# Optimization experiments

Hardware: AMD Instinct MI355X
Metric: run time of the kernel (lower is better)

The kernel has to match this reference:

```python
import jax, jax.numpy as jnp
import numpy as np

B, N, F = 2, 2048, 1024
H, E = 512, 256   # feature_sizes = [1024, 512, 256]
K = 30            # K_max


def setup_inputs() -> dict:
    key = jax.random.key(0)
    k0, k1, k2, k3, k4 = jax.random.split(key, 5)
    x = jax.random.normal(k0, (B, N, F), dtype=jnp.float32)
    s0 = 1.0 / np.sqrt(F)
    s1 = 1.0 / np.sqrt(H)
    # torch.nn.Linear default init: U(-1/sqrt(fan_in), 1/sqrt(fan_in)), weight [out, in]
    W0 = jax.random.uniform(k1, (H, F), jnp.float32, -s0, s0)
    b0 = jax.random.uniform(k2, (H,), jnp.float32, -s0, s0)
    W1 = jax.random.uniform(k3, (E, H), jnp.float32, -s1, s1)
    b1 = jax.random.uniform(k4, (E,), jnp.float32, -s1, s1)
    return {"x": x, "W0": W0, "b0": b0, "W1": W1, "b1": b1}


def _osg_single(xs, W0, b0, W1, b1):
    # xs: [N, F] (no NaNs, so masked_select(~isnan) is identity)
    # DIST (EMBEDDING + cosine)
    h = jax.nn.relu(xs @ W0.T + b0)          # [N, H]
    e = h @ W1.T + b1                         # [N, E]
    corr = e @ e.T                            # [N, N]
    d = jnp.diagonal(corr)                    # [N]
    denom = jnp.sqrt(jnp.clip(d[:, None] * d[None, :], 1e-8, None))
    D = (1.0 - corr / denom) / 2.0            # [N, N]

    # D_SUM_CALC: D_sum[i, j] (j >= i) = sum of D[i:j+1, i:j+1] (block sums)
    # via padded 2D prefix sums. Only the upper triangle is consumed downstream.
    Sp = jnp.pad(jnp.cumsum(jnp.cumsum(D, axis=0), axis=1), ((1, 0), (1, 0)))  # [N+1, N+1]
    dS = jnp.diagonal(Sp)                     # [N+1]
    Bsum = dS[1:][None, :] - Sp[:-1, 1:] - Sp[1:, :-1].T + dS[:-1][:, None]    # [N, N]

    idx = jnp.arange(N)
    BIG = jnp.float32(1e30)
    C0 = Bsum[:, N - 1]                       # C[n, 0] = D_sum[n, N-1]

    # C_TABLE_ALL DP over k, fused with the per-column masked mean:
    # T_pred[i] = mean over all C_all[nn, kk, i] >= 0.
    # k = 0 layer: C_all[n, 0, N-1] = 1 for every n (N entries in column N-1).
    tsum0 = jnp.zeros((N,), jnp.float32).at[N - 1].set(float(N))
    tcnt0 = jnp.zeros((N,), jnp.float32).at[N - 1].set(float(N))

    def step(carry, kk):
        Cprev, tsum, tcnt = carry
        # Cshift[i] = C[i+1, kk-1]; pad value never used (i+1 <= N-kk <= N-1)
        Cshift = jnp.concatenate([Cprev[1:], jnp.zeros((1,), Cprev.dtype)])
        M = Bsum + Cshift[None, :]            # M[nn, i] = D_sum[nn, i] + C[i+1, kk-1]
        valid = (idx[None, :] >= idx[:, None]) & (idx[None, :] < N - kk)  # i in [nn, N-kk)
        Ck = jnp.where(idx < N - kk,
                       jnp.min(jnp.where(valid, M, BIG), axis=1),
                       0.0)                    # torch leaves C at 0 for invalid rows
        soft = jax.nn.softmax(jnp.where(valid, -M, -BIG), axis=1)  # Softmin over valid i
        tsum = tsum + jnp.sum(jnp.where(valid, soft, 0.0), axis=0)
        tcnt = tcnt + jnp.sum(valid, axis=0).astype(tsum.dtype)
        return (Ck, tsum, tcnt), None

    (_, tsum, tcnt), _ = jax.lax.scan(step, (C0, tsum0, tcnt0), jnp.arange(1, K))
    return tsum / tcnt                        # every column has count >= 1 for K >= 2


def reference(x, W0, b0, W1, b1):
    # N == x.shape[1] (no NaN padding needed), so T_out is [B, N]
    return jax.vmap(lambda xs: _osg_single(xs, W0, b0, W1, b1))(x)
```

## Files before the change

### kernel.cpp

```cpp
#include <hip/hip_runtime.h>
#include <hip/hip_bf16.h>
#include <float.h>

#define NTOK 2048
#define FDIM 1024
#define HDIM 512
#define EDIM 256
#define BATCH 2
#define KSEG 30
#define NP1 2049
static const size_t ST2 = (size_t)NP1 * NP1;

__global__ __launch_bounds__(256)
void gemm_nt64(const float* __restrict__ A, int lda,
               const float* __restrict__ Bm, int ldb,
               const float* __restrict__ bias,
               float* __restrict__ C, int ldc, int K)
{
    __shared__ float As[32][68];
    __shared__ float Bs[32][68];
    const int t = threadIdx.x;
    const int tx = t & 15, ty = t >> 4;
    const int lrow = t >> 3, lkv = t & 7;
    const int by = blockIdx.y, bx = blockIdx.x;

    float acc[4][4] = {};
    const int ktiles = K >> 5;
    for (int kt = 0; kt < ktiles; ++kt) {
#pragma unroll
        for (int h = 0; h < 2; ++h) {
            const int r = lrow + h * 32;
            const float4 av = *(const float4*)(A + (size_t)(by * 64 + r) * lda + kt * 32 + lkv * 4);
            As[lkv * 4 + 0][r] = av.x; As[lkv * 4 + 1][r] = av.y;
            As[lkv * 4 + 2][r] = av.z; As[lkv * 4 + 3][r] = av.w;
            const float4 bv = *(const float4*)(Bm + (size_t)(bx * 64 + r) * ldb + kt * 32 + lkv * 4);
            Bs[lkv * 4 + 0][r] = bv.x; Bs[lkv * 4 + 1][r] = bv.y;
            Bs[lkv * 4 + 2][r] = bv.z; Bs[lkv * 4 + 3][r] = bv.w;
        }
        __syncthreads();
#pragma unroll
        for (int kk = 0; kk < 32; ++kk) {
            const float4 a = *(const float4*)&As[kk][ty * 4];
            const float4 b = *(const float4*)&Bs[kk][tx * 4];
            const float ar[4] = {a.x, a.y, a.z, a.w};
            const float br[4] = {b.x, b.y, b.z, b.w};
#pragma unroll
            for (int i = 0; i < 4; ++i)
#pragma unroll
                for (int j = 0; j < 4; ++j)
                    acc[i][j] = fmaf(ar[i], br[j], acc[i][j]);
        }
        __syncthreads();
    }

    const int row0 = by * 64 + ty * 4;
    const int col0 = bx * 64 + tx * 4;
#pragma unroll
    for (int i = 0; i < 4; ++i) {
        float4 v4;
        v4.x = acc[i][0] + bias[col0 + 0];
        v4.y = acc[i][1] + bias[col0 + 1];
        v4.z = acc[i][2] + bias[col0 + 2];
        v4.w = acc[i][3] + bias[col0 + 3];
        *(float4*)(C + (size_t)(row0 + i) * ldc + col0) = v4;
    }
}

__global__ __launch_bounds__(256)
void gemm_nt128s(const float* __restrict__ A, int lda,
                 const float* __restrict__ Bm, int ldb,
                 float* __restrict__ Cp, int ldc, int M, int khalf)
{
    __shared__ float As[16][140];
    __shared__ float Bs[16][140];
    const int t = threadIdx.x;
    const int tx = t & 15, ty = t >> 4;
    const int by = blockIdx.y, bx = blockIdx.x;
    const int k0 = blockIdx.z * khalf;
    const int fq = t & 3, lr = t >> 2;

    float acc[8][8] = {};
    for (int kt = 0; kt < khalf / 16; ++kt) {
#pragma unroll
        for (int h = 0; h < 2; ++h) {
            const int r = lr + h * 64;
            const int rr = r + 4 * (r >> 5);
            const float4 av = *(const float4*)(A + (size_t)(by * 128 + r) * lda + k0 + kt * 16 + fq * 4);
            As[fq * 4 + 0][rr] = av.x; As[fq * 4 + 1][rr] = av.y;
            As[fq * 4 + 2][rr] = av.z; As[fq * 4 + 3][rr] = av.w;
            const float4 bv = *(const float4*)(Bm + (size_t)(bx * 128 + r) * ldb + k0 + kt * 16 + fq * 4);
            Bs[fq * 4 + 0][rr] = bv.x; Bs[fq * 4 + 1][rr] = bv.y;
            Bs[fq * 4 + 2][rr] = bv.z; Bs[fq * 4 + 3][rr] = bv.w;
        }
        __syncthreads();
        const int ma = 8 * ty + 4 * (ty >> 2);
        const int mb = 8 * tx + 4 * (tx >> 2);
#pragma unroll
        for (int k = 0; k < 16; ++k) {
            const float4 a0 = *(const float4*)&As[k][ma];
            const float4 a1 = *(const float4*)&As[k][ma + 4];
            const float4 b0 = *(const float4*)&Bs[k][mb];
            const float4 b1 = *(const float4*)&Bs[k][mb + 4];
            const float ar[8] = {a0.x, a0.y, a0.z, a0.w, a1.x, a1.y, a1.z, a1.w};
            const float br[8] = {b0.x, b0.y, b0.z, b0.w, b1.x, b1.y, b1.z, b1.w};
#pragma unroll
            for (int i = 0; i < 8; ++i)
#pragma unroll
                for (int j = 0; j < 8; ++j)
                    acc[i][j] = fmaf(ar[i], br[j], acc[i][j]);
        }
        __syncthreads();
    }

    float* outp = Cp + (size_t)blockIdx.z * M * ldc;
    const int row0 = by * 128 + ty * 8;
    const int col0 = bx * 128 + tx * 8;
#pragma unroll
    for (int i = 0; i < 8; ++i) {
        float4 w0; w0.x = acc[i][0]; w0.y = acc[i][1]; w0.z = acc[i][2]; w0.w = acc[i][3];
        float4 w1; w1.x = acc[i][4]; w1.y = acc[i][5]; w1.z = acc[i][6]; w1.w = acc[i][7];
        *(float4*)(outp + (size_t)(row0 + i) * ldc + col0) = w0;
        *(float4*)(outp + (size_t)(row0 + i) * ldc + col0 + 4) = w1;
    }
}

__global__ __launch_bounds__(256)
void combine_relu(const float* __restrict__ p0, const float* __restrict__ p1,
                  const float* __restrict__ bias, float* __restrict__ hout)
{
    const int idx = blockIdx.x * 256 + threadIdx.x;
    const float4 a = ((const float4*)p0)[idx];
    const float4 b = ((const float4*)p1)[idx];
    const float4 bs = *(const float4*)&bias[(idx & 127) * 4];
    float4 o;
    o.x = fmaxf(a.x + b.x + bs.x, 0.0f);
    o.y = fmaxf(a.y + b.y + bs.y, 0.0f);
    o.z = fmaxf(a.z + b.z + bs.z, 0.0f);
    o.w = fmaxf(a.w + b.w + bs.w, 0.0f);
    ((float4*)hout)[idx] = o;
}

__global__ __launch_bounds__(256)
void gemm_corr(const float* __restrict__ E, float* __restrict__ D,
               const float* __restrict__ dvec)
{
    __shared__ float As[16][140];
    __shared__ float Bs[16][140];
    const int z = blockIdx.z;
    const float* Eb = E + (size_t)z * NTOK * EDIM;
    float* Db = D + (size_t)z * NTOK * NTOK;
    const int t = threadIdx.x;
    const int tx = t & 15, ty = t >> 4;
    const int by = blockIdx.y, bx = blockIdx.x;
    const int fq = t & 3, lr = t >> 2;

    float acc[8][8] = {};
    for (int kt = 0; kt < EDIM / 16; ++kt) {
#pragma unroll
        for (int h = 0; h < 2; ++h) {
            const int r = lr + h * 64;
            const int rr = r + 4 * (r >> 5);
            const float4 av = *(const float4*)(Eb + (size_t)(by * 128 + r) * EDIM + kt * 16 + fq * 4);
            As[fq * 4 + 0][rr] = av.x; As[fq * 4 + 1][rr] = av.y;
            As[fq * 4 + 2][rr] = av.z; As[fq * 4 + 3][rr] = av.w;
            const float4 bv = *(const float4*)(Eb + (size_t)(bx * 128 + r) * EDIM + kt * 16 + fq * 4);
            Bs[fq * 4 + 0][rr] = bv.x; Bs[fq * 4 + 1][rr] = bv.y;
            Bs[fq * 4 + 2][rr] = bv.z; Bs[fq * 4 + 3][rr] = bv.w;
        }
        __syncthreads();
        const int ma = 8 * ty + 4 * (ty >> 2);
        const int mb = 8 * tx + 4 * (tx >> 2);
#pragma unroll
        for (int k = 0; k < 16; ++k) {
            const float4 a0 = *(const float4*)&As[k][ma];
            const float4 a1 = *(const float4*)&As[k][ma + 4];
            const float4 b0 = *(const float4*)&Bs[k][mb];
            const float4 b1 = *(const float4*)&Bs[k][mb + 4];
            const float ar[8] = {a0.x, a0.y, a0.z, a0.w, a1.x, a1.y, a1.z, a1.w};
            const float br[8] = {b0.x, b0.y, b0.z, b0.w, b1.x, b1.y, b1.z, b1.w};
#pragma unroll
            for (int i = 0; i < 8; ++i)
#pragma unroll
                for (int j = 0; j < 8; ++j)
                    acc[i][j] = fmaf(ar[i], br[j], acc[i][j]);
        }
        __syncthreads();
    }

    const int row0 = by * 128 + ty * 8;
    const int col0 = bx * 128 + tx * 8;
    float di[8], dj[8];
#pragma unroll
    for (int i = 0; i < 8; ++i) di[i] = dvec[z * NTOK + row0 + i];
#pragma unroll
    for (int j = 0; j < 8; ++j) dj[j] = dvec[z * NTOK + col0 + j];
#pragma unroll
    for (int i = 0; i < 8; ++i) {
        float o[8];
#pragma unroll
        for (int j = 0; j < 8; ++j) {
            const float den = sqrtf(fmaxf(di[i] * dj[j], 1e-8f));
            o[j] = 0.5f * (1.0f - acc[i][j] / den);
        }
        float4 w0; w0.x = o[0]; w0.y = o[1]; w0.z = o[2]; w0.w = o[3];
        float4 w1; w1.x = o[4]; w1.y = o[5]; w1.z = o[6]; w1.w = o[7];
        *(float4*)(Db + (size_t)(row0 + i) * NTOK + col0) = w0;
        *(float4*)(Db + (size_t)(row0 + i) * NTOK + col0 + 4) = w1;
    }
}

__global__ __launch_bounds__(256)
void rownorm_kernel(const float* __restrict__ e, float* __restrict__ dvec)
{
    const int wid = (blockIdx.x * 256 + threadIdx.x) >> 6;
    const int lane = threadIdx.x & 63;
    if (wid >= BATCH * NTOK) return;
    const float4 v = *(const float4*)(e + (size_t)wid * EDIM + lane * 4);
    float s = v.x * v.x + v.y * v.y + v.z * v.z + v.w * v.w;
#pragma unroll
    for (int off = 32; off; off >>= 1) s += __shfl_xor(s, off);
    if (lane == 0) dvec[wid] = s;
}

__global__ __launch_bounds__(256)
void sat_row_kernel(const float* __restrict__ D, double* __restrict__ Sp)
{
    const int b = blockIdx.y;
    const int r = blockIdx.x + 1;
    const float* drow = D + (size_t)b * NTOK * NTOK + (size_t)(r - 1) * NTOK;
    double* sprow = Sp + (size_t)b * ST2 + (size_t)r * NP1;
    const int t = threadIdx.x, lane = t & 63, wv = t >> 6;
    __shared__ double wtot[4];
    double carry = 0.0;
    if (t == 0) sprow[0] = 0.0;
    for (int ch = 0; ch < NTOK / 256; ++ch) {
        double v = (double)drow[ch * 256 + t];
#pragma unroll
        for (int d = 1; d < 64; d <<= 1) {
            const double u = __shfl_up(v, (unsigned)d, 64);
            if (lane >= d) v += u;
        }
        if (lane == 63) wtot[wv] = v;
        __syncthreads();
        double pre = carry;
        for (int ww = 0; ww < wv; ++ww) pre += wtot[ww];
        const double tot = carry + wtot[0] + wtot[1] + wtot[2] + wtot[3];
        sprow[ch * 256 + t + 1] = v + pre;
        __syncthreads();
        carry = tot;
    }
}

__global__ void satc1(const double* __restrict__ Sp, double* __restrict__ aux)
{
    const int b = blockIdx.z, s = blockIdx.y;
    const int c = blockIdx.x * 256 + threadIdx.x;
    if (c > NTOK) return;
    const double* sp = Sp + (size_t)b * ST2;
    double tt = 0.0;
    const int r0 = s * 256 + 1;
    for (int r = r0; r < r0 + 256; ++r) tt += sp[(size_t)r * NP1 + c];
    aux[(size_t)(b * 8 + s) * NP1 + c] = tt;
}
__global__ void satc2(double* __restrict__ aux)
{
    const int b = blockIdx.y;
    const int c = blockIdx.x * 256 + threadIdx.x;
    if (c > NTOK) return;
    double run = 0.0;
    for (int s = 0; s < 8; ++s) {
        const size_t id = (size_t)(b * 8 + s) * NP1 + c;
        const double tt = aux[id]; aux[id] = run; run += tt;
    }
}
__global__ void satc3(double* __restrict__ Sp, const double* __restrict__ aux)
{
    const int b = blockIdx.z, s = blockIdx.y;
    const int c = blockIdx.x * 256 + threadIdx.x;
    if (c > NTOK) return;
    double* sp = Sp + (size_t)b * ST2;
    if (s == 0) sp[c] = 0.0;
    double run = aux[(size_t)(b * 8 + s) * NP1 + c];
    const int r0 = s * 256 + 1;
    for (int r = r0; r < r0 + 256; ++r) {
        const size_t id = (size_t)r * NP1 + c;
        run += sp[id];
        sp[id] = run;
    }
}

__global__ void diag_kernel(const double* __restrict__ Sp, double* __restrict__ dg)
{
    const int b = blockIdx.y;
    const int t = blockIdx.x * 256 + threadIdx.x;
    if (t <= NTOK) dg[b * NP1 + t] = Sp[(size_t)b * ST2 + (size_t)t * NP1 + t];
}

__global__ __launch_bounds__(256)
void bsum_kernel(const double* __restrict__ Sp, const double* __restrict__ dg,
                 float* __restrict__ Bsum, float* __restrict__ C0)
{
    const int b = blockIdx.y, i = blockIdx.x;
    const double* sprow = Sp + (size_t)b * ST2 + (size_t)i * NP1;
    const double* dgb = dg + (size_t)b * NP1;
    const double di = dgb[i];
    float* brow = Bsum + (size_t)b * NTOK * NTOK + (size_t)i * NTOK;
    for (int j = i + threadIdx.x; j < NTOK; j += 256) {
        const double v = dgb[j + 1] + di - 2.0 * sprow[j + 1];
        brow[j] = (float)v;
        if (j == NTOK - 1) C0[b * NTOK + i] = (float)v;
    }
}

#define DP_BX 128
#define DP_PAIRS 8
#define RBBIG 3.0e37f

__device__ inline void cstore(float* p, float v)
{
    __hip_atomic_store(p, v, __ATOMIC_RELAXED, __HIP_MEMORY_SCOPE_AGENT);
}

__device__ inline void wait_flags(const int* flagsb, int need)
{
    if (threadIdx.x < DP_BX) {
        const int* f = flagsb + threadIdx.x * 4;
        while (__hip_atomic_load(f, __ATOMIC_RELAXED, __HIP_MEMORY_SCOPE_AGENT) < need)
            __builtin_amdgcn_s_sleep(1);
    }
    __syncthreads();
}

__device__ inline void publish(int* myflag, int val)
{
    asm volatile("s_waitcnt vmcnt(0)" ::: "memory");
    __syncthreads();
    if (threadIdx.x == 0)
        __hip_atomic_store(myflag, val, __ATOMIC_RELAXED, __HIP_MEMORY_SCOPE_AGENT);
}

template<int NC>
__device__ inline void load_rb(const float* __restrict__ brow, int colbase, int lane,
                               float (&rb)[NC])
{
#pragma unroll
    for (int c = 0; c < NC; ++c) {
        const int col = colbase + lane + c * 64;
        rb[c] = (col < NTOK) ? brow[col] : RBBIG;
    }
}

template<int NC>
__device__ inline float pass1(const float (&rb)[NC], const float* __restrict__ cs,
                              int coff, int V, int lane)
{
    float mn = FLT_MAX;
#pragma unroll
    for (int c = 0; c < NC; ++c) {
        const int idx = lane + c * 64;
        if (idx < V) mn = fminf(mn, rb[c] + cs[coff + idx]);
    }
#pragma unroll
    for (int o = 32; o; o >>= 1) mn = fminf(mn, __shfl_xor(mn, o));
    return mn;
}

template<int NC>
__device__ inline void pass2(const float (&rb)[NC], const float* __restrict__ cs,
                             int coff, int V, float mn, int lane, float (&ac)[NC])
{
    float w[NC];
    float s = 0.0f;
#pragma unroll
    for (int c = 0; c < NC; ++c) {
        const int idx = lane + c * 64;
        float x = 0.0f;
        if (idx < V) x = __expf(mn - (rb[c] + cs[coff + idx]));
        w[c] = x;
        s += x;
    }
#pragma unroll
    for (int o = 32; o; o >>= 1) s += __shfl_xor(s, o);
    const float inv = 1.0f / s;
#pragma unroll
    for (int c = 0; c < NC; ++c) ac[c] = __builtin_fmaf(w[c], inv, ac[c]);
}

template<int NC>
__device__ inline void merge_acc(const float (&ac)[NC], int base, int lane,
                                 float* __restrict__ acc_lds)
{
#pragma unroll
    for (int c = 0; c < NC; ++c) {
        const int col = base + lane + c * 64;
        if (col < NTOK && ac[c] != 0.0f) atomicAdd(&acc_lds[col], ac[c]);
    }
}

__global__ __launch_bounds__(256, 1)
void dp_fused_kernel(const float* __restrict__ Bsum,
                     float* __restrict__ Ca, float* __restrict__ Cb,
                     float* __restrict__ tsum, int* __restrict__ flags)
{
    __shared__ float cs[NTOK];
    __shared__ float acc_lds[NTOK];
    const int b = blockIdx.y;
    const int t = threadIdx.x, lane = t & 63, wv = t >> 6;
    const float* Bb = Bsum + (size_t)b * NTOK * NTOK;
    const int pbase = blockIdx.x * DP_PAIRS;
    int* flagsb = flags + b * DP_BX * 4;
    int* myflag = flagsb + blockIdx.x * 4;

    const int p0 = pbase + wv * 2, p1 = p0 + 1;
    const int i1_0 = NTOK - 1 - p0, i1_1 = NTOK - 1 - p1;

    float rbA0[32], rbB0[16], rbA1[32], rbB1[16];
    load_rb<32>(Bb + (size_t)p0 * NTOK, p0, lane, rbA0);
    load_rb<16>(Bb + (size_t)i1_0 * NTOK, i1_0, lane, rbB0);
    load_rb<32>(Bb + (size_t)p1 * NTOK, p1, lane, rbA1);
    load_rb<16>(Bb + (size_t)i1_1 * NTOK, i1_1, lane, rbB1);

    float acA0[32] = {}, acB0[16] = {}, acA1[32] = {}, acB1[16] = {};

    for (int j = t; j < NTOK; j += 256) acc_lds[j] = 0.0f;

    if (t < DP_PAIRS) {
        const int p = pbase + t, i1 = NTOK - 1 - p;
        if (p > 0) cstore(&Ca[b * NTOK + p - 1], Bb[(size_t)p * NTOK + NTOK - 1]);
        cstore(&Ca[b * NTOK + i1 - 1], Bb[(size_t)i1 * NTOK + NTOK - 1]);
    }
    publish(myflag, 0);

    const float* Cr = Ca;
    float* Cn = Cb;

    for (int k = 1; k < KSEG; ++k) {
        wait_flags(flagsb, k - 1);
        {
            const float* base  = Cr + b * NTOK + t * 4;
            const float* base2 = base + 1024;
            float4 va, vb;
            asm volatile(
                "global_load_dwordx4 %0, %2, off sc1\n\t"
                "global_load_dwordx4 %1, %3, off sc1\n\t"
                "s_waitcnt vmcnt(0)"
                : "=&v"(va), "=&v"(vb)
                : "v"(base), "v"(base2)
                : "memory");
            *(float4*)&cs[t * 4] = va;
            *(float4*)&cs[t * 4 + 1024] = vb;
        }
        __syncthreads();
        float* Cnb = Cn + b * NTOK;
        const int jmax = NTOK - k;

        const int VA0 = jmax - p0, VA1 = jmax - p1;
        const int VB0 = p0 + 1 - k, VB1 = p1 + 1 - k;
        const float mnA0 = pass1<32>(rbA0, cs, p0, VA0, lane);
        float mnB0 = 0.0f, mnB1 = 0.0f;
        if (p0 >= k) mnB0 = pass1<16>(rbB0, cs, i1_0, VB0, lane);
        const float mnA1 = pass1<32>(rbA1, cs, p1, VA1, lane);
        if (p1 >= k) mnB1 = pass1<16>(rbB1, cs, i1_1, VB1, lane);
        if (lane == 0) {
            if (p0 > 0) cstore(&Cnb[p0 - 1], mnA0);
            cstore(&Cnb[i1_0 - 1], (p0 >= k) ? mnB0 : 0.0f);
            cstore(&Cnb[p1 - 1], mnA1);
            cstore(&Cnb[i1_1 - 1], (p1 >= k) ? mnB1 : 0.0f);
        }
        publish(myflag, k);

        pass2<32>(rbA0, cs, p0, VA0, mnA0, lane, acA0);
        if (p0 >= k) pass2<16>(rbB0, cs, i1_0, VB0, mnB0, lane, acB0);
        pass2<32>(rbA1, cs, p1, VA1, mnA1, lane, acA1);
        if (p1 >= k) pass2<16>(rbB1, cs, i1_1, VB1, mnB1, lane, acB1);

        float* tmp = (float*)Cr; Cr = Cn; Cn = tmp;
    }

    __syncthreads();
    merge_acc<32>(acA0, p0, lane, acc_lds);
    merge_acc<16>(acB0, i1_0, lane, acc_lds);
    merge_acc<32>(acA1, p1, lane, acc_lds);
    merge_acc<16>(acB1, i1_1, lane, acc_lds);
    __syncthreads();
    float* ts = tsum + b * NTOK;
    for (int j = t; j < NTOK; j += 256) {
        const float v = acc_lds[j];
        if (v != 0.0f) atomicAdd(&ts[j], v);
    }
}

__global__ __launch_bounds__(256)
void dp_step_kernel(const float* __restrict__ Bsum, const float* __restrict__ Cprev,
                    float* __restrict__ Cnext, float* __restrict__ tsum, int kk)
{
    __shared__ float cs[NTOK];
    __shared__ float acc[NTOK];
    const int b = blockIdx.y;
    const int t = threadIdx.x, lane = t & 63, wv = t >> 6;
    const float* Cp = Cprev + b * NTOK;
    for (int j = t; j < NTOK; j += 256) {
        cs[j] = (j < NTOK - 1) ? Cp[j + 1] : 0.0f;
        acc[j] = 0.0f;
    }
    __syncthreads();
    const int jmax = NTOK - kk;
    const int w = blockIdx.x * 4 + wv;
    const float* Bb = Bsum + (size_t)b * NTOK * NTOK;
    float* Cn = Cnext + b * NTOK;
    const int rows[4] = { w, 1023 - w, 1024 + w, 2047 - w };
#pragma unroll
    for (int rr = 0; rr < 4; ++rr) {
        const int i = rows[rr];
        if (i >= jmax) { if (lane == 0) Cn[i] = 0.0f; continue; }
        const float* brow = Bb + (size_t)i * NTOK;
        const int j0 = i + lane;
        float mv[32];
        float mn = FLT_MAX;
#pragma unroll
        for (int c = 0; c < 32; ++c) {
            const int j = j0 + c * 64;
            float v = FLT_MAX;
            if (j < jmax) v = brow[j] + cs[j];
            mv[c] = v;
            mn = fminf(mn, v);
        }
#pragma unroll
        for (int off = 32; off; off >>= 1) mn = fminf(mn, __shfl_xor(mn, off));
        if (lane == 0) Cn[i] = mn;
        float s = 0.0f;
#pragma unroll
        for (int c = 0; c < 32; ++c) {
            const int j = j0 + c * 64;
            float p = 0.0f;
            if (j < jmax) p = __expf(mn - mv[c]);
            mv[c] = p;
            s += p;
        }
#pragma unroll
        for (int off = 32; off; off >>= 1) s += __shfl_xor(s, off);
        const float inv = 1.0f / s;
#pragma unroll
        for (int c = 0; c < 32; ++c) {
            const int j = j0 + c * 64;
            if (j < jmax) atomicAdd(&acc[j], mv[c] * inv);
        }
    }
    __syncthreads();
    float* ts = tsum + b * NTOK;
    for (int j = t; j < NTOK; j += 256) {
        const float v = acc[j];
        if (v != 0.0f) atomicAdd(&ts[j], v);
    }
}

__global__ void finalize_kernel(const float* __restrict__ tsum, float* __restrict__ out)
{
    const int b = blockIdx.y;
    const int j = blockIdx.x * 256 + threadIdx.x;
    if (j >= NTOK) return;
    float ts = tsum[b * NTOK + j];
    int steps = NTOK - 1 - j;
    if (steps > KSEG - 1) steps = KSEG - 1;
    float tc = (float)(j + 1) * (float)steps;
    if (j == NTOK - 1) { ts += (float)NTOK; tc += (float)NTOK; }
    out[b * NTOK + j] = ts / tc;
}

extern "C" void kernel_launch(void* const* d_in, const int* in_sizes, int n_in,
                              void* d_out, int out_size, void* d_ws, size_t ws_size,
                              hipStream_t stream)
{
    const float* x  = (const float*)d_in[0];
    const float* W0 = (const float*)d_in[1];
    const float* b0 = (const float*)d_in[2];
    const float* W1 = (const float*)d_in[3];
    const float* b1 = (const float*)d_in[4];
    float* out = (float*)d_out;

    char* ws = (char*)d_ws;
    size_t off = 0;
    auto alloc = [&](size_t bytes) -> void* {
        void* p = (void*)(ws + off);
        off += (bytes + 255) & ~(size_t)255;
        return p;
    };
    double* Sp   = (double*)alloc((size_t)BATCH * ST2 * sizeof(double));
    float*  Dm   = (float*) alloc((size_t)BATCH * NTOK * NTOK * sizeof(float));
    float*  h    = (float*) alloc((size_t)BATCH * NTOK * HDIM * sizeof(float));
    float*  e    = (float*) alloc((size_t)BATCH * NTOK * EDIM * sizeof(float));
    float*  dvec = (float*) alloc((size_t)BATCH * NTOK * sizeof(float));
    double* dg   = (double*)alloc((size_t)BATCH * NP1 * sizeof(double));
    double* aux  = (double*)alloc((size_t)BATCH * 8 * NP1 * sizeof(double));
    float*  CA   = (float*) alloc((size_t)BATCH * NTOK * sizeof(float));
    float*  CB   = (float*) alloc((size_t)BATCH * NTOK * sizeof(float));
    float*  tsum = (float*) alloc((size_t)BATCH * NTOK * sizeof(float));
    int*    flags= (int*)   alloc((size_t)BATCH * DP_BX * 4 * sizeof(int));
    (void)ws_size; (void)in_sizes; (void)n_in; (void)out_size;

    hipMemsetAsync(tsum, 0, (size_t)BATCH * NTOK * sizeof(float), stream);
    hipMemsetAsync(flags, 0xFF, (size_t)BATCH * DP_BX * 4 * sizeof(int), stream);

    float* Hpart = Dm;
    gemm_nt128s<<<dim3(HDIM / 128, (BATCH * NTOK) / 128, 2), 256, 0, stream>>>(
        x, FDIM, W0, FDIM, Hpart, HDIM, BATCH * NTOK, FDIM / 2);
    combine_relu<<<dim3((BATCH * NTOK * HDIM / 4) / 256), 256, 0, stream>>>(
        Hpart, Hpart + (size_t)BATCH * NTOK * HDIM, b0, h);
    gemm_nt64<<<dim3(EDIM / 64, (BATCH * NTOK) / 64), 256, 0, stream>>>(
        h, HDIM, W1, HDIM, b1, e, EDIM, HDIM);
    rownorm_kernel<<<dim3((BATCH * NTOK) / 4), 256, 0, stream>>>(e, dvec);
    gemm_corr<<<dim3(NTOK / 128, NTOK / 128, BATCH), 256, 0, stream>>>(e, Dm, dvec);
    sat_row_kernel<<<dim3(NTOK, BATCH), 256, 0, stream>>>(Dm, Sp);
    satc1<<<dim3((NP1 + 255) / 256, 8, BATCH), 256, 0, stream>>>(Sp, aux);
    satc2<<<dim3((NP1 + 255) / 256, BATCH), 256, 0, stream>>>(aux);
    satc3<<<dim3((NP1 + 255) / 256, 8, BATCH), 256, 0, stream>>>(Sp, aux);
    diag_kernel<<<dim3((NP1 + 255) / 256, BATCH), 256, 0, stream>>>(Sp, dg);
    bsum_kernel<<<dim3(NTOK, BATCH), 256, 0, stream>>>(Sp, dg, Dm, CA);

    void* args[] = { (void*)&Dm, (void*)&CA, (void*)&CB, (void*)&tsum, (void*)&flags };
    hipError_t err = hipLaunchCooperativeKernel((const void*)dp_fused_kernel,
                                                dim3(DP_BX, BATCH), dim3(256),
                                                args, 0, stream);
    if (err != hipSuccess) {
        float* cp = CA; float* cn = CB;
        for (int kk = 1; kk < KSEG; ++kk) {
            dp_step_kernel<<<dim3(128, BATCH), 256, 0, stream>>>(Dm, cp, cn, tsum, kk);
            float* tmp = cp; cp = cn; cn = tmp;
        }
    }
    finalize_kernel<<<dim3(NTOK / 256, BATCH), 256, 0, stream>>>(tsum, out);
}
```

Measured before the change: 739.4 us.

## Fuse column prefix pass with block-sum computation and skip lower-triangle work

Stops writing the full 2D prefix-sum table back to memory. The column scan is merged into the Bsum kernel, which computes each Bsum[r][c-1] directly from its running column sum. A separate kernel computes only the diagonal, and blocks entirely below the diagonal are skipped in the column-partial and fused passes. This removes a full read-modify-write of the large double-precision table plus a separate Bsum read pass. The cost is column-major strided Bsum writes, which may coalesce poorly.

```diff
diff --git a/kernel.cpp b/kernel.cpp
--- a/kernel.cpp
+++ b/kernel.cpp
@@ -223,16 +223,16 @@
 }
 
 __global__ __launch_bounds__(256)
-void sat_row_kernel(const float* __restrict__ D, double* __restrict__ Sp)
+void sat_row_kernel(const float* __restrict__ D, double* __restrict__ R)
 {
     const int b = blockIdx.y;
     const int r = blockIdx.x + 1;
     const float* drow = D + (size_t)b * NTOK * NTOK + (size_t)(r - 1) * NTOK;
-    double* sprow = Sp + (size_t)b * ST2 + (size_t)r * NP1;
+    double* rrow = R + (size_t)b * ST2 + (size_t)r * NP1;
     const int t = threadIdx.x, lane = t & 63, wv = t >> 6;
     __shared__ double wtot[4];
     double carry = 0.0;
-    if (t == 0) sprow[0] = 0.0;
+    if (t == 0) rrow[0] = 0.0;
     for (int ch = 0; ch < NTOK / 256; ++ch) {
         double v = (double)drow[ch * 256 + t];
 #pragma unroll
@@ -245,21 +245,22 @@
         double pre = carry;
         for (int ww = 0; ww < wv; ++ww) pre += wtot[ww];
         const double tot = carry + wtot[0] + wtot[1] + wtot[2] + wtot[3];
-        sprow[ch * 256 + t + 1] = v + pre;
+        rrow[ch * 256 + t + 1] = v + pre;
         __syncthreads();
         carry = tot;
     }
 }
 
-__global__ void satc1(const double* __restrict__ Sp, double* __restrict__ aux)
-{
-    const int b = blockIdx.z, s = blockIdx.y;
-    const int c = blockIdx.x * 256 + threadIdx.x;
+__global__ void satc1(const double* __restrict__ R, double* __restrict__ aux)
+{
+    const int b = blockIdx.z, s = blockIdx.y, cb = blockIdx.x;
+    if (cb < s) return;
+    const int c = cb * 256 + threadIdx.x;
     if (c > NTOK) return;
-    const double* sp = Sp + (size_t)b * ST2;
+    const double* rb = R + (size_t)b * ST2;
     double tt = 0.0;
     const int r0 = s * 256 + 1;
-    for (int r = r0; r < r0 + 256; ++r) tt += sp[(size_t)r * NP1 + c];
+    for (int r = r0; r < r0 + 256; ++r) tt += rb[(size_t)r * NP1 + c];
     aux[(size_t)(b * 8 + s) * NP1 + c] = tt;
 }
 __global__ void satc2(double* __restrict__ aux)
@@ -273,42 +274,50 @@
         const double tt = aux[id]; aux[id] = run; run += tt;
     }
 }
-__global__ void satc3(double* __restrict__ Sp, const double* __restrict__ aux)
-{
-    const int b = blockIdx.z, s = blockIdx.y;
+__global__ void satc_diag(const double* __restrict__ R, const double* __restrict__ aux,
+                          double* __restrict__ dg)
+{
+    const int b = blockIdx.y;
     const int c = blockIdx.x * 256 + threadIdx.x;
     if (c > NTOK) return;
-    double* sp = Sp + (size_t)b * ST2;
-    if (s == 0) sp[c] = 0.0;
+    if (c == 0) { dg[b * NP1] = 0.0; return; }
+    const int s = (c - 1) >> 8;
+    const int r0 = s * 256 + 1;
+    const double* rb = R + (size_t)b * ST2;
     double run = aux[(size_t)(b * 8 + s) * NP1 + c];
+    for (int r = r0; r <= c; ++r)
+        run += rb[(size_t)r * NP1 + c];
+    dg[b * NP1 + c] = run;
+}
+__global__ __launch_bounds__(256)
+void satc3_bsum(const double* __restrict__ R, const double* __restrict__ aux,
+                const double* __restrict__ dg,
+                float* __restrict__ Bsum, float* __restrict__ C0)
+{
+    const int b = blockIdx.z, s = blockIdx.y, cb = blockIdx.x;
     const int r0 = s * 256 + 1;
-    for (int r = r0; r < r0 + 256; ++r) {
-        const size_t id = (size_t)r * NP1 + c;
-        run += sp[id];
-        sp[id] = run;
-    }
-}
-
-__global__ void diag_kernel(const double* __restrict__ Sp, double* __restrict__ dg)
-{
-    const int b = blockIdx.y;
-    const int t = blockIdx.x * 256 + threadIdx.x;
-    if (t <= NTOK) dg[b * NP1 + t] = Sp[(size_t)b * ST2 + (size_t)t * NP1 + t];
-}
-
-__global__ __launch_bounds__(256)
-void bsum_kernel(const double* __restrict__ Sp, const double* __restrict__ dg,
-                 float* __restrict__ Bsum, float* __restrict__ C0)
-{
-    const int b = blockIdx.y, i = blockIdx.x;
-    const double* sprow = Sp + (size_t)b * ST2 + (size_t)i * NP1;
-    const double* dgb = dg + (size_t)b * NP1;
-    const double di = dgb[i];
-    float* brow = Bsum + (size_t)b * NTOK * NTOK + (size_t)i * NTOK;
-    for (int j = i + threadIdx.x; j < NTOK; j += 256) {
-        const double v = dgb[j + 1] + di - 2.0 * sprow[j + 1];
-        brow[j] = (float)v;
-        if (j == NTOK - 1) C0[b * NTOK + i] = (float)v;
+    if (r0 >= (cb + 1) * 256) return;
+    const int c = cb * 256 + threadIdx.x;
+    if (c > NTOK || c == 0) return;
+    const double* rb = R + (size_t)b * ST2;
+    const double* dgb = dg + b * NP1;
+    const double dgc = dgb[c];
+    float* Bb = Bsum + (size_t)b * NTOK * NTOK;
+    float* C0b = C0 + b * NTOK;
+    if (s == 0) {
+        const float v0 = (float)dgc;
+        Bb[c - 1] = v0;
+        if (c == NTOK) C0b[0] = v0;
+    }
+    double run = aux[(size_t)(b * 8 + s) * NP1 + c];
+    const int rend = r0 + 256;
+    for (int r = r0; r < rend; ++r) {
+        run += rb[(size_t)r * NP1 + c];
+        if (r < c) {
+            const float v = (float)(dgc + dgb[r] - 2.0 * run);
+            Bb[(size_t)r * NTOK + (c - 1)] = v;
+            if (c == NTOK) C0b[r] = v;
+        }
     }
 }
 
@@ -585,7 +594,7 @@
         off += (bytes + 255) & ~(size_t)255;
         return p;
     };
-    double* Sp   = (double*)alloc((size_t)BATCH * ST2 * sizeof(double));
+    double* Rsc  = (double*)alloc((size_t)BATCH * ST2 * sizeof(double));
     float*  Dm   = (float*) alloc((size_t)BATCH * NTOK * NTOK * sizeof(float));
     float*  h    = (float*) alloc((size_t)BATCH * NTOK * HDIM * sizeof(float));
     float*  e    = (float*) alloc((size_t)BATCH * NTOK * EDIM * sizeof(float));
@@ -610,12 +619,12 @@
         h, HDIM, W1, HDIM, b1, e, EDIM, HDIM);
     rownorm_kernel<<<dim3((BATCH * NTOK) / 4), 256, 0, stream>>>(e, dvec);
     gemm_corr<<<dim3(NTOK / 128, NTOK / 128, BATCH), 256, 0, stream>>>(e, Dm, dvec);
-    sat_row_kernel<<<dim3(NTOK, BATCH), 256, 0, stream>>>(Dm, Sp);
-    satc1<<<dim3((NP1 + 255) / 256, 8, BATCH), 256, 0, stream>>>(Sp, aux);
+    sat_row_kernel<<<dim3(NTOK, BATCH), 256, 0, stream>>>(Dm, Rsc);
+    satc1<<<dim3((NP1 + 255) / 256, 8, BATCH), 256, 0, stream>>>(Rsc, aux);
     satc2<<<dim3((NP1 + 255) / 256, BATCH), 256, 0, stream>>>(aux);
-    satc3<<<dim3((NP1 + 255) / 256, 8, BATCH), 256, 0, stream>>>(Sp, aux);
-    diag_kernel<<<dim3((NP1 + 255) / 256, BATCH), 256, 0, stream>>>(Sp, dg);
-    bsum_kernel<<<dim3(NTOK, BATCH), 256, 0, stream>>>(Sp, dg, Dm, CA);
+    satc_diag<<<dim3((NP1 + 255) / 256, BATCH), 256, 0, stream>>>(Rsc, aux, dg);
+    satc3_bsum<<<dim3((NP1 + 255) / 256, 8, BATCH), 256, 0, stream>>>(
+        Rsc, aux, dg, Dm, CA);
 
     void* args[] = { (void*)&Dm, (void*)&CA, (void*)&CB, (void*)&tsum, (void*)&flags };
     hipError_t err = hipLaunchCooperativeKernel((const void*)dp_fused_kernel,
```

New measurement: 803.5 us. 1.09x slower.
